# Performance work log

Hardware: AMD Instinct MI355X
Metric: run time of the kernel (lower is better)

The kernel has to match this reference:

```python
import jax, jax.numpy as jnp
import numpy as np

INPUT_DIM = 1024
EMBED_DIM = 1024
NUM_HEADS = 16
HEAD_DIM = EMBED_DIM // NUM_HEADS


def _xavier_uniform(key, shape):
    fan_in, fan_out = shape[1], shape[0]
    limit = float(np.sqrt(6.0 / (fan_in + fan_out)))
    return jax.random.uniform(key, shape, jnp.float32, -limit, limit)


def setup_inputs() -> dict:
    key = jax.random.key(0)
    kx, kqkv, ko = jax.random.split(key, 3)
    x = jax.random.normal(kx, (2, 2048, INPUT_DIM), jnp.float32)
    # torch Linear stores weight as [out, in]; we keep that convention
    w_qkv = _xavier_uniform(kqkv, (3 * EMBED_DIM, INPUT_DIM))
    b_qkv = jnp.zeros((3 * EMBED_DIM,), jnp.float32)
    w_o = _xavier_uniform(ko, (EMBED_DIM, EMBED_DIM))
    b_o = jnp.zeros((EMBED_DIM,), jnp.float32)
    return {"x": x, "w_qkv": w_qkv, "b_qkv": b_qkv, "w_o": w_o, "b_o": b_o}


def reference(x, w_qkv, b_qkv, w_o, b_o):
    B, S, _ = x.shape
    H, D = NUM_HEADS, HEAD_DIM
    qkv = jnp.einsum("bsi,oi->bso", x, w_qkv) + b_qkv          # [B,S,3E]
    qkv = qkv.reshape(B, S, H, 3 * D).transpose(0, 2, 1, 3)    # [B,H,S,3D]
    q, k, v = jnp.split(qkv, 3, axis=-1)                        # each [B,H,S,D]
    scores = jnp.einsum("bhqd,bhkd->bhqk", q, k) / jnp.sqrt(jnp.float32(D))
    attn = jax.nn.softmax(scores, axis=-1)                      # [B,H,S,S]
    vals = jnp.einsum("bhqk,bhkd->bhqd", attn, v)               # [B,H,S,D]
    vals = vals.transpose(0, 2, 1, 3).reshape(B, S, H * D)      # [B,S,E]
    return jnp.einsum("bse,oe->bso", vals, w_o) + b_o
```

## Files before the change

### kernel.cpp

```cpp
#include <hip/hip_runtime.h>
#include <hip/hip_bf16.h>


typedef __attribute__((ext_vector_type(8))) short bf16x8;
typedef __attribute__((ext_vector_type(4))) short bf16x4;
typedef __attribute__((ext_vector_type(4))) float f32x4;

#define MFMA16(a, b, c) __builtin_amdgcn_mfma_f32_16x16x32_bf16((a), (b), (c), 0, 0, 0)

#if __has_builtin(__builtin_amdgcn_exp2f)
#define EXP2F(x) __builtin_amdgcn_exp2f(x)
#else
#define EXP2F(x) exp2f(x)
#endif

static __device__ __forceinline__ unsigned short f2bf_bits(float v) {
    __hip_bfloat16 h = __float2bfloat16(v);
    return *reinterpret_cast<unsigned short*>(&h);
}

static __device__ __forceinline__ bf16x8 cvt8(const float* p) {
    const f32x4 a = reinterpret_cast<const f32x4*>(p)[0];
    const f32x4 b = reinterpret_cast<const f32x4*>(p)[1];
    bf16x8 r;
    r[0] = (short)f2bf_bits(a[0]); r[1] = (short)f2bf_bits(a[1]);
    r[2] = (short)f2bf_bits(a[2]); r[3] = (short)f2bf_bits(a[3]);
    r[4] = (short)f2bf_bits(b[0]); r[5] = (short)f2bf_bits(b[1]);
    r[6] = (short)f2bf_bits(b[2]); r[7] = (short)f2bf_bits(b[3]);
    return r;
}

__device__ __forceinline__ bf16x8 ldg8(const __hip_bfloat16* p) {
    return *reinterpret_cast<const bf16x8*>(p);
}

__device__ __forceinline__ void load16_lds(const __hip_bfloat16* g, unsigned short* l) {
    __builtin_amdgcn_global_load_lds(
        (const __attribute__((address_space(1))) void*)g,
        (__attribute__((address_space(3))) void*)l, 16, 0, 0);
}

__global__ __launch_bounds__(256)
void cast2_f32_bf16(const float* __restrict__ x, __hip_bfloat16* __restrict__ xb,
                    const float* __restrict__ w, __hip_bfloat16* __restrict__ wb) {
    const int bid = blockIdx.x;
    const float* src = (bid < 512) ? x : w;
    __hip_bfloat16* dst = (bid < 512) ? xb : wb;
    const int rb = (bid < 512) ? bid : (bid - 512);
    const size_t base = (size_t)rb * 8192 + (size_t)threadIdx.x * 32;
#pragma unroll
    for (int i = 0; i < 4; ++i)
        *reinterpret_cast<bf16x8*>(dst + base + i * 8) = cvt8(src + base + i * 8);
}

__global__ __launch_bounds__(256)
void cast_f32_bf16(const float* __restrict__ src, __hip_bfloat16* __restrict__ dst) {
    const size_t base = ((size_t)blockIdx.x * 256 + threadIdx.x) * 32;
#pragma unroll
    for (int i = 0; i < 4; ++i)
        *reinterpret_cast<bf16x8*>(dst + base + i * 8) = cvt8(src + base + i * 8);
}

__global__ __launch_bounds__(256)
void qkv_gemm(const __hip_bfloat16* __restrict__ xb,
              const __hip_bfloat16* __restrict__ wb,
              const float* __restrict__ bqkv,
              __hip_bfloat16* __restrict__ Q,
              __hip_bfloat16* __restrict__ K,
              __hip_bfloat16* __restrict__ Vt) {
    __shared__ unsigned short As[2][128 * 32];
    __shared__ unsigned short Bs[2][128 * 32];

    const int tid  = threadIdx.x;
    const int lane = tid & 63;
    const int wv   = tid >> 6;
    const int quad = lane >> 4;
    const int l16  = lane & 15;
    const int wm   = wv >> 1;
    const int wn   = wv & 1;

    const int bid = blockIdx.x;
    const int xcd = bid & 7;
    const int r   = bid >> 3;
    const int m0  = (r / 3) * 128;
    const int n0  = (xcd * 3 + (r % 3)) * 128;

    const __hip_bfloat16* agl = xb + (size_t)(m0 + wv * 32 + (lane >> 2)) * 1024 + (lane & 3) * 8;
    const __hip_bfloat16* bgl = wb + (size_t)(n0 + wv * 32 + (lane >> 2)) * 1024 + (lane & 3) * 8;

    f32x4 zv = {0.f, 0.f, 0.f, 0.f};
    f32x4 acc[4][4];
#pragma unroll
    for (int ii = 0; ii < 4; ++ii)
#pragma unroll
        for (int jj = 0; jj < 4; ++jj) acc[ii][jj] = zv;

    load16_lds(agl, &As[0][(wv * 32) * 32]);
    load16_lds(agl + 16 * 1024, &As[0][(wv * 32 + 16) * 32]);
    load16_lds(bgl, &Bs[0][(wv * 32) * 32]);
    load16_lds(bgl + 16 * 1024, &Bs[0][(wv * 32 + 16) * 32]);
    __syncthreads();

    for (int k0 = 0; k0 < 1024; k0 += 32) {
        const int p = (k0 >> 5) & 1;
        if (k0 + 32 < 1024) {
            const int q = p ^ 1;
            load16_lds(agl + k0 + 32, &As[q][(wv * 32) * 32]);
            load16_lds(agl + 16 * 1024 + k0 + 32, &As[q][(wv * 32 + 16) * 32]);
            load16_lds(bgl + k0 + 32, &Bs[q][(wv * 32) * 32]);
            load16_lds(bgl + 16 * 1024 + k0 + 32, &Bs[q][(wv * 32 + 16) * 32]);
        }
        bf16x8 af[4], bf[4];
#pragma unroll
        for (int ii = 0; ii < 4; ++ii)
            af[ii] = *reinterpret_cast<const bf16x8*>(
                &As[p][(wm * 64 + ii * 16 + l16) * 32 + quad * 8]);
#pragma unroll
        for (int jj = 0; jj < 4; ++jj)
            bf[jj] = *reinterpret_cast<const bf16x8*>(
                &Bs[p][(wn * 64 + jj * 16 + l16) * 32 + quad * 8]);
#pragma unroll
        for (int ii = 0; ii < 4; ++ii)
#pragma unroll
            for (int jj = 0; jj < 4; ++jj)
                acc[ii][jj] = MFMA16(af[ii], bf[jj], acc[ii][jj]);
        __syncthreads();
    }

    const float QSCALE = 0.18033688011f;

#pragma unroll
    for (int jj = 0; jj < 4; ++jj) {
        const int n = n0 + wn * 64 + jj * 16 + l16;
        const float bias = bqkv[n];
        const int h = n / 192;
        const int r2 = n - h * 192;
        const int t = r2 >> 6;
        const int d = r2 & 63;
#pragma unroll
        for (int ii = 0; ii < 4; ++ii) {
            const int mb = m0 + wm * 64 + ii * 16 + quad * 4;
            const int b = mb >> 11;
            const int s0 = mb & 2047;
            const int bh = b * 16 + h;
            if (t == 2) {
                bf16x4 pk;
#pragma unroll
                for (int i = 0; i < 4; ++i)
                    pk[i] = (short)f2bf_bits(acc[ii][jj][i] + bias);
                *reinterpret_cast<bf16x4*>(&Vt[((size_t)bh * 64 + d) * 2048 + s0]) = pk;
            } else {
#pragma unroll
                for (int i = 0; i < 4; ++i) {
                    const float v = acc[ii][jj][i] + bias;
                    if (t == 0)
                        Q[((size_t)bh * 2048 + s0 + i) * 64 + d] = __float2bfloat16(v * QSCALE);
                    else
                        K[((size_t)bh * 2048 + s0 + i) * 64 + d] = __float2bfloat16(v);
                }
            }
        }
    }
}

__global__ __launch_bounds__(256)
void attn_kernel(const __hip_bfloat16* __restrict__ Q,
                 const __hip_bfloat16* __restrict__ K,
                 const __hip_bfloat16* __restrict__ Vt,
                 __hip_bfloat16* __restrict__ AO) {
    __shared__ unsigned short Ks0[2][32 * 40];
    __shared__ unsigned short Ks1[2][32 * 40];
    __shared__ unsigned short Vs[2][64 * 40];

    const int tid  = threadIdx.x;
    const int lane = tid & 63;
    const int wv   = tid >> 6;
    const int quad = lane >> 4;
    const int l16  = lane & 15;

    const int blk = blockIdx.x;
    const int xcd = blk & 7;
    const int sub = blk >> 3;
    const int bh  = xcd * 4 + (sub & 3);
    const int qb  = sub >> 2;
    const int q0  = qb * 128 + wv * 32;
    const int b   = bh >> 4;
    const int h   = bh & 15;

    const __hip_bfloat16* Qp = Q  + (size_t)bh * 131072;
    const __hip_bfloat16* Kp = K  + (size_t)bh * 131072;
    const __hip_bfloat16* Vp = Vt + (size_t)bh * 131072;

    bf16x8 bQ[2][2];
#pragma unroll
    for (int t = 0; t < 2; ++t)
#pragma unroll
        for (int dh = 0; dh < 2; ++dh)
            bQ[t][dh] = ldg8(Qp + (size_t)(q0 + t * 16 + l16) * 64 + dh * 32 + quad * 8);

    const int kr = tid >> 3;
    const int kc = (tid & 7) * 8;
    const int kb = kr & 7;
    const int sig = (kb < 4) ? ((kr >> 3) * 4 + kb) : (16 + (kr >> 3) * 4 + (kb - 4));
    const int koff = (kc < 32) ? (sig * 40 + kc) : (sig * 40 + (kc - 32));
    const int kis1 = (kc >= 32);
    const int vr = tid >> 2;
    const int vc = (tid & 3) * 8;
    const int voff = vr * 40 + vc;

    const __hip_bfloat16* kgp = Kp + (size_t)kr * 64 + kc;
    const __hip_bfloat16* vgp = Vp + (size_t)vr * 2048 + vc;

    f32x4 zv = {0.f, 0.f, 0.f, 0.f};
    f32x4 Of[2][4];
#pragma unroll
    for (int t = 0; t < 2; ++t)
#pragma unroll
        for (int jj = 0; jj < 4; ++jj) Of[t][jj] = zv;
    float li[2] = {0.f, 0.f};

    bf16x8 gk = ldg8(kgp);
    bf16x8 gv = ldg8(vgp);
    {
        unsigned short* kw0 = kis1 ? &Ks1[0][koff] : &Ks0[0][koff];
        *reinterpret_cast<bf16x8*>(kw0) = gk;
        *reinterpret_cast<bf16x8*>(&Vs[0][voff]) = gv;
    }
    gk = ldg8(kgp + (size_t)32 * 64);
    gv = ldg8(vgp + 32);
    __syncthreads();

    for (int kt = 0; kt < 64; ++kt) {
        const int p = kt & 1;
        if (kt < 63) {
            unsigned short* kw1 = kis1 ? &Ks1[p ^ 1][koff] : &Ks0[p ^ 1][koff];
            *reinterpret_cast<bf16x8*>(kw1) = gk;
            *reinterpret_cast<bf16x8*>(&Vs[p ^ 1][voff]) = gv;
        }
        if (kt < 62) {
            gk = ldg8(kgp + (size_t)(kt + 2) * 32 * 64);
            gv = ldg8(vgp + (kt + 2) * 32);
        }

        const bf16x8 aKA0 = *reinterpret_cast<const bf16x8*>(&Ks0[p][l16 * 40 + quad * 8]);
        const bf16x8 aKA1 = *reinterpret_cast<const bf16x8*>(&Ks1[p][l16 * 40 + quad * 8]);
        const bf16x8 aKB0 = *reinterpret_cast<const bf16x8*>(&Ks0[p][(16 + l16) * 40 + quad * 8]);
        const bf16x8 aKB1 = *reinterpret_cast<const bf16x8*>(&Ks1[p][(16 + l16) * 40 + quad * 8]);
        bf16x8 aV[4];
#pragma unroll
        for (int jj = 0; jj < 4; ++jj)
            aV[jj] = *reinterpret_cast<const bf16x8*>(&Vs[p][(jj * 16 + l16) * 40 + quad * 8]);

        f32x4 sA[2], sB[2];
#pragma unroll
        for (int t = 0; t < 2; ++t) {
            sA[t] = zv; sB[t] = zv;
            sA[t] = MFMA16(aKA0, bQ[t][0], sA[t]);
            sA[t] = MFMA16(aKA1, bQ[t][1], sA[t]);
            sB[t] = MFMA16(aKB0, bQ[t][0], sB[t]);
            sB[t] = MFMA16(aKB1, bQ[t][1], sB[t]);
        }

#pragma unroll
        for (int t = 0; t < 2; ++t) {
            float pA[4], pB[4];
#pragma unroll
            for (int i = 0; i < 4; ++i) {
                pA[i] = EXP2F(sA[t][i]);
                pB[i] = EXP2F(sB[t][i]);
            }
            li[t] += ((pA[0] + pA[1]) + (pA[2] + pA[3]))
                   + ((pB[0] + pB[1]) + (pB[2] + pB[3]));

            bf16x8 bP;
            bP[0] = (short)f2bf_bits(pA[0]); bP[1] = (short)f2bf_bits(pA[1]);
            bP[2] = (short)f2bf_bits(pA[2]); bP[3] = (short)f2bf_bits(pA[3]);
            bP[4] = (short)f2bf_bits(pB[0]); bP[5] = (short)f2bf_bits(pB[1]);
            bP[6] = (short)f2bf_bits(pB[2]); bP[7] = (short)f2bf_bits(pB[3]);

#pragma unroll
            for (int jj = 0; jj < 4; ++jj)
                Of[t][jj] = MFMA16(aV[jj], bP, Of[t][jj]);
        }
        __syncthreads();
    }

#pragma unroll
    for (int t = 0; t < 2; ++t) {
        li[t] += __shfl_xor(li[t], 16);
        li[t] += __shfl_xor(li[t], 32);
    }

#pragma unroll
    for (int t = 0; t < 2; ++t) {
        const float linv = 1.f / li[t];
        const int s = q0 + t * 16 + l16;
        __hip_bfloat16* aop = AO + (((size_t)b * 2048 + s) * 16 + h) * 64;
#pragma unroll
        for (int jj = 0; jj < 4; ++jj) {
            bf16x4 pk;
#pragma unroll
            for (int i = 0; i < 4; ++i)
                pk[i] = (short)f2bf_bits(Of[t][jj][i] * linv);
            *reinterpret_cast<bf16x4*>(aop + jj * 16 + quad * 4) = pk;
        }
    }
}

__global__ __launch_bounds__(256)
void out_gemm(const __hip_bfloat16* __restrict__ A,
              const __hip_bfloat16* __restrict__ wob,
              const float* __restrict__ bo,
              float* __restrict__ out) {
    __shared__ unsigned short As[2][64 * 32];
    __shared__ unsigned short Bs[2][128 * 32];

    const int tid  = threadIdx.x;
    const int lane = tid & 63;
    const int wv   = tid >> 6;
    const int quad = lane >> 4;
    const int l16  = lane & 15;
    const int wm   = wv >> 1;
    const int wn   = wv & 1;

    const int bid = blockIdx.x;
    const int m0  = (bid >> 3) * 64;
    const int n0  = (bid & 7) * 128;

    const __hip_bfloat16* agl = A   + (size_t)(m0 + wv * 16 + (lane >> 2)) * 1024 + (lane & 3) * 8;
    const __hip_bfloat16* bgl = wob + (size_t)(n0 + wv * 32 + (lane >> 2)) * 1024 + (lane & 3) * 8;

    f32x4 zv = {0.f, 0.f, 0.f, 0.f};
    f32x4 acc[2][4];
#pragma unroll
    for (int ii = 0; ii < 2; ++ii)
#pragma unroll
        for (int jj = 0; jj < 4; ++jj) acc[ii][jj] = zv;

    load16_lds(agl, &As[0][(wv * 16) * 32]);
    load16_lds(bgl, &Bs[0][(wv * 32) * 32]);
    load16_lds(bgl + 16 * 1024, &Bs[0][(wv * 32 + 16) * 32]);
    __syncthreads();

    for (int k0 = 0; k0 < 1024; k0 += 32) {
        const int p = (k0 >> 5) & 1;
        if (k0 + 32 < 1024) {
            const int q = p ^ 1;
            load16_lds(agl + k0 + 32, &As[q][(wv * 16) * 32]);
            load16_lds(bgl + k0 + 32, &Bs[q][(wv * 32) * 32]);
            load16_lds(bgl + 16 * 1024 + k0 + 32, &Bs[q][(wv * 32 + 16) * 32]);
        }
        bf16x8 af[2], bf[4];
#pragma unroll
        for (int ii = 0; ii < 2; ++ii)
            af[ii] = *reinterpret_cast<const bf16x8*>(
                &As[p][(wm * 32 + ii * 16 + l16) * 32 + quad * 8]);
#pragma unroll
        for (int jj = 0; jj < 4; ++jj)
            bf[jj] = *reinterpret_cast<const bf16x8*>(
                &Bs[p][(wn * 64 + jj * 16 + l16) * 32 + quad * 8]);
#pragma unroll
        for (int ii = 0; ii < 2; ++ii)
#pragma unroll
            for (int jj = 0; jj < 4; ++jj)
                acc[ii][jj] = MFMA16(af[ii], bf[jj], acc[ii][jj]);
        __syncthreads();
    }

#pragma unroll
    for (int jj = 0; jj < 4; ++jj) {
        const int n = n0 + wn * 64 + jj * 16 + l16;
        const float bias = bo[n];
#pragma unroll
        for (int ii = 0; ii < 2; ++ii) {
#pragma unroll
            for (int i = 0; i < 4; ++i) {
                const int m = m0 + wm * 32 + ii * 16 + quad * 4 + i;
                out[(size_t)m * 1024 + n] = acc[ii][jj][i] + bias;
            }
        }
    }
}

extern "C" void kernel_launch(void* const* d_in, const int* in_sizes, int n_in,
                              void* d_out, int out_size, void* d_ws, size_t ws_size,
                              hipStream_t stream) {
    const float* x    = (const float*)d_in[0];
    const float* wqkv = (const float*)d_in[1];
    const float* bqkv = (const float*)d_in[2];
    const float* wo   = (const float*)d_in[3];
    const float* bo   = (const float*)d_in[4];
    float* out = (float*)d_out;

    __hip_bfloat16* ws = (__hip_bfloat16*)d_ws;
    __hip_bfloat16* Q   = ws;
    __hip_bfloat16* K   = ws + (size_t)4194304;
    __hip_bfloat16* Vt  = ws + (size_t)8388608;
    __hip_bfloat16* AO  = ws + (size_t)12582912;
    __hip_bfloat16* wob = Q;

    __hip_bfloat16* xb     = (__hip_bfloat16*)d_out;
    __hip_bfloat16* wqkvb  = xb + (size_t)4194304;

    cast2_f32_bf16<<<dim3(896), 256, 0, stream>>>(x, xb, wqkv, wqkvb);
    qkv_gemm<<<dim3(768), 256, 0, stream>>>(xb, wqkvb, bqkv, Q, K, Vt);
    attn_kernel<<<dim3(512), 256, 0, stream>>>(Q, K, Vt, AO);
    cast_f32_bf16<<<dim3(128), 256, 0, stream>>>(wo, wob);
    out_gemm<<<dim3(512), 256, 0, stream>>>(AO, wob, bo, out);
}
```

Measured before the change: 199.1 us.

## Split attention block into eight waves of sixteen queries each

Each attention wave now processes 16 query rows instead of 32, and the block grows to 512 threads so each block still covers 128 queries. K and V tile staging is reassigned so half the waves load K and half load V. The aim is more resident waves to hide MFMA/exp latency with fewer registers per wave. The cost is half the reuse of each LDS-loaded K/V fragment and more LDS read traffic per query.

```diff
diff --git a/kernel.cpp b/kernel.cpp
--- a/kernel.cpp
+++ b/kernel.cpp
@@ -163,7 +163,7 @@
     }
 }
 
-__global__ __launch_bounds__(256)
+__global__ __launch_bounds__(512, 4)
 void attn_kernel(const __hip_bfloat16* __restrict__ Q,
                  const __hip_bfloat16* __restrict__ K,
                  const __hip_bfloat16* __restrict__ Vt,
@@ -183,7 +183,7 @@
     const int sub = blk >> 3;
     const int bh  = xcd * 4 + (sub & 3);
     const int qb  = sub >> 2;
-    const int q0  = qb * 128 + wv * 32;
+    const int q0  = qb * 128 + wv * 16;
     const int b   = bh >> 4;
     const int h   = bh & 15;
 
@@ -191,56 +191,51 @@
     const __hip_bfloat16* Kp = K  + (size_t)bh * 131072;
     const __hip_bfloat16* Vp = Vt + (size_t)bh * 131072;
 
-    bf16x8 bQ[2][2];
-#pragma unroll
-    for (int t = 0; t < 2; ++t)
-#pragma unroll
-        for (int dh = 0; dh < 2; ++dh)
-            bQ[t][dh] = ldg8(Qp + (size_t)(q0 + t * 16 + l16) * 64 + dh * 32 + quad * 8);
-
-    const int kr = tid >> 3;
-    const int kc = (tid & 7) * 8;
-    const int kb = kr & 7;
-    const int sig = (kb < 4) ? ((kr >> 3) * 4 + kb) : (16 + (kr >> 3) * 4 + (kb - 4));
-    const int koff = (kc < 32) ? (sig * 40 + kc) : (sig * 40 + (kc - 32));
-    const int kis1 = (kc >= 32);
-    const int vr = tid >> 2;
-    const int vc = (tid & 3) * 8;
-    const int voff = vr * 40 + vc;
-
-    const __hip_bfloat16* kgp = Kp + (size_t)kr * 64 + kc;
-    const __hip_bfloat16* vgp = Vp + (size_t)vr * 2048 + vc;
+    bf16x8 bQ[2];
+#pragma unroll
+    for (int dh = 0; dh < 2; ++dh)
+        bQ[dh] = ldg8(Qp + (size_t)(q0 + l16) * 64 + dh * 32 + quad * 8);
+
+    unsigned short* s0;
+    unsigned short* s1;
+    const __hip_bfloat16* sgp;
+    size_t sstep;
+    if (wv < 4) {
+        const int half   = wv >> 1;
+        const int rowblk = wv & 1;
+        const int krow   = rowblk * 16 + l16;
+        const int keyg   = (l16 >> 2) * 8 + rowblk * 4 + (l16 & 3);
+        sgp   = Kp + (size_t)keyg * 64 + half * 32 + quad * 8;
+        unsigned short* base0 = half ? &Ks1[0][0] : &Ks0[0][0];
+        unsigned short* base1 = half ? &Ks1[1][0] : &Ks0[1][0];
+        s0 = base0 + krow * 40 + quad * 8;
+        s1 = base1 + krow * 40 + quad * 8;
+        sstep = 32 * 64;
+    } else {
+        const int vrow = (wv - 4) * 16 + l16;
+        sgp   = Vp + (size_t)vrow * 2048 + quad * 8;
+        s0 = &Vs[0][vrow * 40 + quad * 8];
+        s1 = &Vs[1][vrow * 40 + quad * 8];
+        sstep = 32;
+    }
 
     f32x4 zv = {0.f, 0.f, 0.f, 0.f};
-    f32x4 Of[2][4];
-#pragma unroll
-    for (int t = 0; t < 2; ++t)
-#pragma unroll
-        for (int jj = 0; jj < 4; ++jj) Of[t][jj] = zv;
-    float li[2] = {0.f, 0.f};
-
-    bf16x8 gk = ldg8(kgp);
-    bf16x8 gv = ldg8(vgp);
-    {
-        unsigned short* kw0 = kis1 ? &Ks1[0][koff] : &Ks0[0][koff];
-        *reinterpret_cast<bf16x8*>(kw0) = gk;
-        *reinterpret_cast<bf16x8*>(&Vs[0][voff]) = gv;
-    }
-    gk = ldg8(kgp + (size_t)32 * 64);
-    gv = ldg8(vgp + 32);
+    f32x4 Of[4];
+#pragma unroll
+    for (int jj = 0; jj < 4; ++jj) Of[jj] = zv;
+    float li = 0.f;
+
+    bf16x8 g = ldg8(sgp);
+    *reinterpret_cast<bf16x8*>(s0) = g;
+    g = ldg8(sgp + sstep);
     __syncthreads();
 
     for (int kt = 0; kt < 64; ++kt) {
         const int p = kt & 1;
-        if (kt < 63) {
-            unsigned short* kw1 = kis1 ? &Ks1[p ^ 1][koff] : &Ks0[p ^ 1][koff];
-            *reinterpret_cast<bf16x8*>(kw1) = gk;
-            *reinterpret_cast<bf16x8*>(&Vs[p ^ 1][voff]) = gv;
-        }
-        if (kt < 62) {
-            gk = ldg8(kgp + (size_t)(kt + 2) * 32 * 64);
-            gv = ldg8(vgp + (kt + 2) * 32);
-        }
+        if (kt < 63)
+            *reinterpret_cast<bf16x8*>(p ? s0 : s1) = g;
+        if (kt < 62)
+            g = ldg8(sgp + (size_t)(kt + 2) * sstep);
 
         const bf16x8 aKA0 = *reinterpret_cast<const bf16x8*>(&Ks0[p][l16 * 40 + quad * 8]);
         const bf16x8 aKA1 = *reinterpret_cast<const bf16x8*>(&Ks1[p][l16 * 40 + quad * 8]);
@@ -251,57 +246,47 @@
         for (int jj = 0; jj < 4; ++jj)
             aV[jj] = *reinterpret_cast<const bf16x8*>(&Vs[p][(jj * 16 + l16) * 40 + quad * 8]);
 
-        f32x4 sA[2], sB[2];
-#pragma unroll
-        for (int t = 0; t < 2; ++t) {
-            sA[t] = zv; sB[t] = zv;
-            sA[t] = MFMA16(aKA0, bQ[t][0], sA[t]);
-            sA[t] = MFMA16(aKA1, bQ[t][1], sA[t]);
-            sB[t] = MFMA16(aKB0, bQ[t][0], sB[t]);
-            sB[t] = MFMA16(aKB1, bQ[t][1], sB[t]);
-        }
-
-#pragma unroll
-        for (int t = 0; t < 2; ++t) {
-            float pA[4], pB[4];
-#pragma unroll
-            for (int i = 0; i < 4; ++i) {
-                pA[i] = EXP2F(sA[t][i]);
-                pB[i] = EXP2F(sB[t][i]);
-            }
-            li[t] += ((pA[0] + pA[1]) + (pA[2] + pA[3]))
-                   + ((pB[0] + pB[1]) + (pB[2] + pB[3]));
-
-            bf16x8 bP;
-            bP[0] = (short)f2bf_bits(pA[0]); bP[1] = (short)f2bf_bits(pA[1]);
-            bP[2] = (short)f2bf_bits(pA[2]); bP[3] = (short)f2bf_bits(pA[3]);
-            bP[4] = (short)f2bf_bits(pB[0]); bP[5] = (short)f2bf_bits(pB[1]);
-            bP[6] = (short)f2bf_bits(pB[2]); bP[7] = (short)f2bf_bits(pB[3]);
-
-#pragma unroll
-            for (int jj = 0; jj < 4; ++jj)
-                Of[t][jj] = MFMA16(aV[jj], bP, Of[t][jj]);
-        }
+        f32x4 sA = zv, sB = zv;
+        sA = MFMA16(aKA0, bQ[0], sA);
+        sA = MFMA16(aKA1, bQ[1], sA);
+        sB = MFMA16(aKB0, bQ[0], sB);
+        sB = MFMA16(aKB1, bQ[1], sB);
+
+        float pA[4], pB[4];
+#pragma unroll
+        for (int i = 0; i < 4; ++i) {
+            pA[i] = EXP2F(sA[i]);
+            pB[i] = EXP2F(sB[i]);
+        }
+        li += ((pA[0] + pA[1]) + (pA[2] + pA[3]))
+            + ((pB[0] + pB[1]) + (pB[2] + pB[3]));
+
+        bf16x8 bP;
+        bP[0] = (short)f2bf_bits(pA[0]); bP[1] = (short)f2bf_bits(pA[1]);
+        bP[2] = (short)f2bf_bits(pA[2]); bP[3] = (short)f2bf_bits(pA[3]);
+        bP[4] = (short)f2bf_bits(pB[0]); bP[5] = (short)f2bf_bits(pB[1]);
+        bP[6] = (short)f2bf_bits(pB[2]); bP[7] = (short)f2bf_bits(pB[3]);
+
+#pragma unroll
+        for (int jj = 0; jj < 4; ++jj)
+            Of[jj] = MFMA16(aV[jj], bP, Of[jj]);
+
         __syncthreads();
     }
 
-#pragma unroll
-    for (int t = 0; t < 2; ++t) {
-        li[t] += __shfl_xor(li[t], 16);
-        li[t] += __shfl_xor(li[t], 32);
-    }
-
-#pragma unroll
-    for (int t = 0; t < 2; ++t) {
-        const float linv = 1.f / li[t];
-        const int s = q0 + t * 16 + l16;
+    li += __shfl_xor(li, 16);
+    li += __shfl_xor(li, 32);
+
+    {
+        const float linv = 1.f / li;
+        const int s = q0 + l16;
         __hip_bfloat16* aop = AO + (((size_t)b * 2048 + s) * 16 + h) * 64;
 #pragma unroll
         for (int jj = 0; jj < 4; ++jj) {
             bf16x4 pk;
 #pragma unroll
             for (int i = 0; i < 4; ++i)
-                pk[i] = (short)f2bf_bits(Of[t][jj][i] * linv);
+                pk[i] = (short)f2bf_bits(Of[jj][i] * linv);
             *reinterpret_cast<bf16x4*>(aop + jj * 16 + quad * 4) = pk;
         }
     }
@@ -404,7 +389,7 @@
 
     cast2_f32_bf16<<<dim3(896), 256, 0, stream>>>(x, xb, wqkv, wqkvb);
     qkv_gemm<<<dim3(768), 256, 0, stream>>>(xb, wqkvb, bqkv, Q, K, Vt);
-    attn_kernel<<<dim3(512), 256, 0, stream>>>(Q, K, Vt, AO);
+    attn_kernel<<<dim3(512), 512, 0, stream>>>(Q, K, Vt, AO);
     cast_f32_bf16<<<dim3(128), 256, 0, stream>>>(wo, wob);
     out_gemm<<<dim3(512), 256, 0, stream>>>(AO, wob, bo, out);
 }
```

After: 196.7 us. No clear change (-1.2%).

## Store K/V tiles in LDS in MFMA fragment order for contiguous reads

Applied to the files above, without the earlier changes.

Replaces the padded row-major K and V shared-memory tiles with a single buffer laid out in MFMA fragment order. Each thread writes its global load straight to a linear slot, and each lane reads operands from contiguous 16-byte slots, which removes address arithmetic and bank-conflict padding. It also adds a min-blocks-per-CU hint of 4 to launch_bounds, which may constrain register allocation. Correctness depends on the key permutation (keyg) matching the fragment layout the old sigma mapping produced.

```diff
diff --git a/kernel.cpp b/kernel.cpp
--- a/kernel.cpp
+++ b/kernel.cpp
@@ -163,14 +163,12 @@
     }
 }
 
-__global__ __launch_bounds__(256)
+__global__ __launch_bounds__(256, 4)
 void attn_kernel(const __hip_bfloat16* __restrict__ Q,
                  const __hip_bfloat16* __restrict__ K,
                  const __hip_bfloat16* __restrict__ Vt,
                  __hip_bfloat16* __restrict__ AO) {
-    __shared__ unsigned short Ks0[2][32 * 40];
-    __shared__ unsigned short Ks1[2][32 * 40];
-    __shared__ unsigned short Vs[2][64 * 40];
+    __shared__ unsigned short SB[2][4096];
 
     const int tid  = threadIdx.x;
     const int lane = tid & 63;
@@ -198,18 +196,14 @@
         for (int dh = 0; dh < 2; ++dh)
             bQ[t][dh] = ldg8(Qp + (size_t)(q0 + t * 16 + l16) * 64 + dh * 32 + quad * 8);
 
-    const int kr = tid >> 3;
-    const int kc = (tid & 7) * 8;
-    const int kb = kr & 7;
-    const int sig = (kb < 4) ? ((kr >> 3) * 4 + kb) : (16 + (kr >> 3) * 4 + (kb - 4));
-    const int koff = (kc < 32) ? (sig * 40 + kc) : (sig * 40 + (kc - 32));
-    const int kis1 = (kc >= 32);
-    const int vr = tid >> 2;
-    const int vc = (tid & 3) * 8;
-    const int voff = vr * 40 + vc;
-
-    const __hip_bfloat16* kgp = Kp + (size_t)kr * 64 + kc;
-    const __hip_bfloat16* vgp = Vp + (size_t)vr * 2048 + vc;
+    const int kf   = wv;
+    const int keyg = (l16 >> 2) * 8 + (l16 & 3) + ((kf >> 1) << 2);
+    const int kd0  = (kf & 1) * 32 + quad * 8;
+    const __hip_bfloat16* ksrc = Kp + (size_t)keyg * 64 + kd0;
+    const __hip_bfloat16* vsrc = Vp + (size_t)(wv * 16 + l16) * 2048 + quad * 8;
+
+    unsigned short* kd[2] = { &SB[0][tid * 8],        &SB[1][tid * 8] };
+    unsigned short* vd[2] = { &SB[0][tid * 8 + 2048], &SB[1][tid * 8 + 2048] };
 
     f32x4 zv = {0.f, 0.f, 0.f, 0.f};
     f32x4 Of[2][4];
@@ -219,37 +213,34 @@
         for (int jj = 0; jj < 4; ++jj) Of[t][jj] = zv;
     float li[2] = {0.f, 0.f};
 
-    bf16x8 gk = ldg8(kgp);
-    bf16x8 gv = ldg8(vgp);
-    {
-        unsigned short* kw0 = kis1 ? &Ks1[0][koff] : &Ks0[0][koff];
-        *reinterpret_cast<bf16x8*>(kw0) = gk;
-        *reinterpret_cast<bf16x8*>(&Vs[0][voff]) = gv;
-    }
-    gk = ldg8(kgp + (size_t)32 * 64);
-    gv = ldg8(vgp + 32);
+    bf16x8 gk = ldg8(ksrc);
+    bf16x8 gv = ldg8(vsrc);
+    *reinterpret_cast<bf16x8*>(kd[0]) = gk;
+    *reinterpret_cast<bf16x8*>(vd[0]) = gv;
+    gk = ldg8(ksrc + 2048);
+    gv = ldg8(vsrc + 32);
     __syncthreads();
 
     for (int kt = 0; kt < 64; ++kt) {
         const int p = kt & 1;
         if (kt < 63) {
-            unsigned short* kw1 = kis1 ? &Ks1[p ^ 1][koff] : &Ks0[p ^ 1][koff];
-            *reinterpret_cast<bf16x8*>(kw1) = gk;
-            *reinterpret_cast<bf16x8*>(&Vs[p ^ 1][voff]) = gv;
+            *reinterpret_cast<bf16x8*>(kd[p ^ 1]) = gk;
+            *reinterpret_cast<bf16x8*>(vd[p ^ 1]) = gv;
         }
         if (kt < 62) {
-            gk = ldg8(kgp + (size_t)(kt + 2) * 32 * 64);
-            gv = ldg8(vgp + (kt + 2) * 32);
-        }
-
-        const bf16x8 aKA0 = *reinterpret_cast<const bf16x8*>(&Ks0[p][l16 * 40 + quad * 8]);
-        const bf16x8 aKA1 = *reinterpret_cast<const bf16x8*>(&Ks1[p][l16 * 40 + quad * 8]);
-        const bf16x8 aKB0 = *reinterpret_cast<const bf16x8*>(&Ks0[p][(16 + l16) * 40 + quad * 8]);
-        const bf16x8 aKB1 = *reinterpret_cast<const bf16x8*>(&Ks1[p][(16 + l16) * 40 + quad * 8]);
+            gk = ldg8(ksrc + (size_t)(kt + 2) * 2048);
+            gv = ldg8(vsrc + (size_t)(kt + 2) * 32);
+        }
+
+        const unsigned short* base = &SB[p][lane * 8];
+        const bf16x8 aKA0 = *reinterpret_cast<const bf16x8*>(base + 0 * 512);
+        const bf16x8 aKA1 = *reinterpret_cast<const bf16x8*>(base + 1 * 512);
+        const bf16x8 aKB0 = *reinterpret_cast<const bf16x8*>(base + 2 * 512);
+        const bf16x8 aKB1 = *reinterpret_cast<const bf16x8*>(base + 3 * 512);
         bf16x8 aV[4];
 #pragma unroll
         for (int jj = 0; jj < 4; ++jj)
-            aV[jj] = *reinterpret_cast<const bf16x8*>(&Vs[p][(jj * 16 + l16) * 40 + quad * 8]);
+            aV[jj] = *reinterpret_cast<const bf16x8*>(base + (4 + jj) * 512);
 
         f32x4 sA[2], sB[2];
 #pragma unroll
```

After: 197.4 us. About the same (-0.9%).
